# Kernel tuning notes

Measured on AMD Instinct MI355X. Metric: run time of the kernel, lower is better.

The kernel has to match this reference:

```python
import jax, jax.numpy as jnp
import numpy as np

B, N, IN_C, HID, K1, K2, OUT_C = 128, 512, 128, 32, 100, 10, 10
E_PER = 8192  # edges per graph (avg degree 16)
EPS = 1e-15


def _lin(key, fan_in, fan_out):
    return jax.random.normal(key, (fan_in, fan_out), jnp.float32) / np.sqrt(fan_in)


def setup_inputs() -> dict:
    key = jax.random.key(0)
    ks = jax.random.split(key, 20)
    total = B * N
    x = jax.random.normal(ks[0], (total, IN_C), jnp.float32)
    # per-graph random edges, offset into the global node index space
    src_l = jax.random.randint(ks[1], (B, E_PER), 0, N)
    dst_l = jax.random.randint(ks[2], (B, E_PER), 0, N)
    off = (jnp.arange(B, dtype=jnp.int32) * N)[:, None]
    edge_index = jnp.stack([(src_l + off).reshape(-1), (dst_l + off).reshape(-1)]).astype(jnp.int32)
    batch = (jnp.arange(total, dtype=jnp.int32) // N).astype(jnp.int32)
    return {
        "x": x,
        "edge_index": edge_index,
        "batch": batch,
        "conv1_W": _lin(ks[3], IN_C, HID), "conv1_b": jnp.zeros((HID,), jnp.float32),
        "pool1_W": _lin(ks[4], HID, K1), "pool1_b": jnp.zeros((K1,), jnp.float32),
        "conv2_rel_W": _lin(ks[5], HID, HID), "conv2_rel_b": jnp.zeros((HID,), jnp.float32),
        "conv2_root_W": _lin(ks[6], HID, HID),
        "pool2_W": _lin(ks[7], HID, K2), "pool2_b": jnp.zeros((K2,), jnp.float32),
        "conv3_rel_W": _lin(ks[8], HID, HID), "conv3_rel_b": jnp.zeros((HID,), jnp.float32),
        "conv3_root_W": _lin(ks[9], HID, HID),
        "lin1_W": _lin(ks[10], HID, HID), "lin1_b": jnp.zeros((HID,), jnp.float32),
        "lin2_W": _lin(ks[11], HID, OUT_C), "lin2_b": jnp.zeros((OUT_C,), jnp.float32),
    }


def gcn_conv(x, edge_index, W, b):
    # GCNConv with add_self_loops=True, symmetric normalization
    total = x.shape[0]
    loops = jnp.arange(total, dtype=edge_index.dtype)
    src = jnp.concatenate([edge_index[0], loops])
    dst = jnp.concatenate([edge_index[1], loops])
    w = jnp.ones(src.shape[0], x.dtype)
    deg = jax.ops.segment_sum(w, dst, num_segments=total)
    dis = jnp.where(deg > 0, jax.lax.rsqrt(deg), 0.0)
    norm = dis[src] * dis[dst]
    xw = x @ W
    out = jax.ops.segment_sum(norm[:, None] * xw[src], dst, num_segments=total)
    return out + b


def dense_mincut_pool(x, adj, s, mask=None):
    # x:[b,n,f] adj:[b,n,n] s:[b,n,k]
    s = jax.nn.softmax(s, axis=-1)
    if mask is not None:
        m = mask[..., None].astype(x.dtype)
        x = x * m
        s = s * m
    out = jnp.einsum('bnk,bnf->bkf', s, x)
    out_adj = jnp.einsum('bnk,bnm,bml->bkl', s, adj, s)
    mincut_num = jnp.trace(out_adj, axis1=-2, axis2=-1)
    d_flat = adj.sum(-1)  # [b,n]
    mincut_den = jnp.einsum('bnk,bn,bnk->b', s, d_flat, s)  # trace(s^T D s)
    mincut_loss = jnp.mean(-(mincut_num / mincut_den))
    k = s.shape[-1]
    ss = jnp.einsum('bnk,bnl->bkl', s, s)
    ss_norm = jnp.linalg.norm(ss, axis=(-1, -2), keepdims=True)
    i_s = jnp.eye(k, dtype=x.dtype) / jnp.sqrt(jnp.asarray(k, x.dtype))  # I_k / ||I_k||_F
    ortho_loss = jnp.mean(jnp.linalg.norm(ss / ss_norm - i_s, axis=(-1, -2)))
    # zero diagonal then symmetric degree-normalize
    out_adj = out_adj * (1.0 - jnp.eye(k, dtype=x.dtype))
    d = jnp.sqrt(out_adj.sum(-1))[..., None] + EPS
    out_adj = out_adj / d / jnp.swapaxes(d, -1, -2)
    return out, out_adj, mincut_loss, ortho_loss


def dense_graph_conv(x, adj, rel_W, rel_b, root_W):
    # DenseGraphConv(aggr='add'): lin_rel(adj @ x) + lin_root(x)
    return (adj @ x) @ rel_W + rel_b + x @ root_W


def reference(x, edge_index, batch, conv1_W, conv1_b, pool1_W, pool1_b,
              conv2_rel_W, conv2_rel_b, conv2_root_W, pool2_W, pool2_b,
              conv3_rel_W, conv3_rel_b, conv3_root_W, lin1_W, lin1_b, lin2_W, lin2_b):
    h = jax.nn.relu(gcn_conv(x, edge_index, conv1_W, conv1_b))
    # to_dense_batch: sorted batch with N nodes per graph -> reshape; mask all-true
    xd = h.reshape(B, N, HID)
    mask = jnp.ones((B, N), bool)
    # to_dense_adj
    b_idx = edge_index[0] // N
    s_l = edge_index[0] % N
    d_l = edge_index[1] % N
    adj = jnp.zeros((B, N, N), x.dtype).at[b_idx, s_l, d_l].add(1.0)
    s = xd @ pool1_W + pool1_b
    xd, adj, mc1, o1 = dense_mincut_pool(xd, adj, s, mask)
    xd = jax.nn.relu(dense_graph_conv(xd, adj, conv2_rel_W, conv2_rel_b, conv2_root_W))
    s = xd @ pool2_W + pool2_b
    xd, adj, mc2, o2 = dense_mincut_pool(xd, adj, s)
    xd = dense_graph_conv(xd, adj, conv3_rel_W, conv3_rel_b, conv3_root_W)
    g = xd.mean(axis=1)  # [B, HID]
    g = jax.nn.relu(g @ lin1_W + lin1_b)
    g = g @ lin2_W + lin2_b
    return jax.nn.log_softmax(g, axis=-1), mc1 + mc2 + o1 + o2
```

## Files before the change

kernel.cpp:

```cpp
#include <hip/hip_runtime.h>
#include <hip/hip_bf16.h>

#define TB   128
#define NN   512
#define INC  128
#define HH   32
#define KP1  100
#define KP2  10
#define OC   10
#define EPER 8192
#define NT   (TB*NN)
#define ET   (TB*EPER)
#define ZTR  264
#define ZTS  40
#define XTS  136

typedef unsigned int  u32;
typedef unsigned short u16;
typedef __attribute__((ext_vector_type(8))) short bf16x8;
typedef __attribute__((ext_vector_type(16))) float f32x16;

__device__ __forceinline__ u32 bfr(float f) {
    u32 b = __float_as_uint(f);
    return (b + 0x7fffu + ((b >> 16) & 1u)) >> 16;
}
__device__ __forceinline__ u32 pk2(float a, float b) { return bfr(a) | (bfr(b) << 16); }
__device__ __forceinline__ float blo(u32 u) { return __uint_as_float(u << 16); }
__device__ __forceinline__ float bhi(u32 u) { return __uint_as_float(u & 0xffff0000u); }

__global__ __launch_bounds__(1024) void k_pre(const int* __restrict__ ei,
                                              int* __restrict__ cnt_src, int* __restrict__ cnt_dst,
                                              int* __restrict__ off_src, int* __restrict__ off_dst,
                                              u16* __restrict__ srt_dst, u16* __restrict__ srt_src,
                                              float* __restrict__ dis, float* __restrict__ aux,
                                              const float* __restrict__ x, const float* __restrict__ W,
                                              u16* __restrict__ xwb, float* __restrict__ out) {
    __shared__ __align__(16) u16 sX[512 * XTS];
    __shared__ __align__(16) u16 sW[32 * XTS];
    int tid = threadIdx.x, b = blockIdx.x;
    if (b < TB) {
        int* hs = (int*)sX;
        int* hd = hs + NN;
        int* ps = hd + NN;
        int* pd = ps + NN;
        u16* sdl = (u16*)(pd + NN);
        u16* ssl = sdl + EPER;
        int g = b, goff = g * NN;
        if (tid == 0) aux[g] = 0.f;
        if (g == 0 && tid == 0) out[1280] = 0.f;
        if (tid < NN) { hs[tid] = 0; hd[tid] = 0; }
        __syncthreads();
        const int* es = ei + (size_t)g * EPER;
        const int* ed = ei + ET + (size_t)g * EPER;
        for (int e = tid; e < EPER; e += 1024) {
            atomicAdd(&hs[es[e] - goff], 1);
            atomicAdd(&hd[ed[e] - goff], 1);
        }
        __syncthreads();
        int vs = 0, vd = 0;
        if (tid < NN) { vs = hs[tid]; vd = hd[tid]; ps[tid] = vs; pd[tid] = vd; }
        __syncthreads();
        for (int off = 1; off < NN; off <<= 1) {
            int xa = 0, xb = 0;
            if (tid < NN) {
                xa = ps[tid]; xb = pd[tid];
                if (tid >= off) { xa += ps[tid - off]; xb += pd[tid - off]; }
            }
            __syncthreads();
            if (tid < NN) { ps[tid] = xa; pd[tid] = xb; }
            __syncthreads();
        }
        int eso = 0, edo = 0;
        if (tid < NN) {
            eso = ps[tid] - vs; edo = pd[tid] - vd;
            cnt_src[goff + tid] = vs;  cnt_dst[goff + tid] = vd;
            off_src[goff + tid] = g * EPER + eso;
            off_dst[goff + tid] = g * EPER + edo;
            dis[goff + tid] = rsqrtf(1.0f + (float)vd);
        }
        __syncthreads();
        if (tid < NN) { ps[tid] = eso; pd[tid] = edo; }
        __syncthreads();
        for (int e = tid; e < EPER; e += 1024) {
            int s = es[e] - goff, d = ed[e] - goff;
            int p = atomicAdd(&ps[s], 1); sdl[p] = (u16)d;
            int q = atomicAdd(&pd[d], 1); ssl[q] = (u16)s;
        }
        __syncthreads();
        u32* wd = (u32*)(srt_dst + (size_t)g * EPER);
        u32* ws = (u32*)(srt_src + (size_t)g * EPER);
        const u32* rd = (const u32*)sdl;
        const u32* rs = (const u32*)ssl;
        for (int i = tid; i < EPER / 2; i += 1024) { wd[i] = rd[i]; ws[i] = rs[i]; }
        return;
    }
    int nbase = (b - TB) * 512;
    for (int i = tid; i < INC * HH; i += 1024) {
        int k = i >> 5, n = i & 31;
        sW[n * XTS + k] = (u16)bfr(W[i]);
    }
    for (int i = tid; i < 512 * 32; i += 1024) {
        int r = i >> 5, q = i & 31;
        float4 v = ((const float4*)(x + (size_t)(nbase + r) * INC))[q];
        u32* dst = (u32*)&sX[r * XTS + q * 4];
        dst[0] = pk2(v.x, v.y);
        dst[1] = pk2(v.z, v.w);
    }
    __syncthreads();
    int wave = tid >> 6, lane = tid & 63;
    int lc = lane & 31, half = lane >> 5;
    f32x16 acc;
#pragma unroll
    for (int r = 0; r < 16; r++) acc[r] = 0.f;
#pragma unroll
    for (int kc = 0; kc < 8; kc++) {
        bf16x8 af  = *(const bf16x8*)&sX[(wave * 32 + lc) * XTS + kc * 16 + half * 8];
        bf16x8 bfv = *(const bf16x8*)&sW[lc * XTS + kc * 16 + half * 8];
        acc = __builtin_amdgcn_mfma_f32_32x32x16_bf16(af, bfv, acc, 0, 0, 0);
    }
#pragma unroll
    for (int r = 0; r < 16; r++) {
        int m = (r & 3) + 8 * (r >> 2) + 4 * half;
        int rowg = nbase + wave * 32 + m;
        xwb[(size_t)rowg * HH + lc] = (u16)bfr(acc[r]);
    }
}

__global__ __launch_bounds__(256) void k_gcng(const u16* __restrict__ ssrc, const int* __restrict__ od,
                                              const int* __restrict__ cd, const u32* __restrict__ xwb32,
                                              const float* __restrict__ dis, const float* __restrict__ bias,
                                              u32* __restrict__ hb32) {
    int tid = threadIdx.x;
    int b = blockIdx.x;
    int r8 = b & 7, j = b >> 3;
    int g = r8 + 8 * (j & 15);
    int chunk = j >> 4;
    int n = g * NN + chunk * 16 + (tid >> 4), cp = tid & 15;
    int goff = g * NN;
    int base = od[n], cnt = cd[n];
    float dn = dis[n];
    u32 us = xwb32[(size_t)n * 16 + cp];
    float a0 = dn * blo(us), a1 = dn * bhi(us);
    int i = 0;
    for (; i + 4 <= cnt; i += 4) {
        int s0 = goff + ssrc[base + i],     s1v = goff + ssrc[base + i + 1];
        int s2 = goff + ssrc[base + i + 2], s3  = goff + ssrc[base + i + 3];
        float d0 = dis[s0], d1 = dis[s1v], d2 = dis[s2], d3 = dis[s3];
        u32 u0 = xwb32[(size_t)s0 * 16 + cp];
        u32 u1 = xwb32[(size_t)s1v * 16 + cp];
        u32 u2 = xwb32[(size_t)s2 * 16 + cp];
        u32 u3 = xwb32[(size_t)s3 * 16 + cp];
        a0 += d0 * blo(u0) + d1 * blo(u1) + d2 * blo(u2) + d3 * blo(u3);
        a1 += d0 * bhi(u0) + d1 * bhi(u1) + d2 * bhi(u2) + d3 * bhi(u3);
    }
    for (; i < cnt; i++) {
        int s0 = goff + ssrc[base + i]; float d0 = dis[s0];
        u32 u0 = xwb32[(size_t)s0 * 16 + cp];
        a0 += d0 * blo(u0); a1 += d0 * bhi(u0);
    }
    float v0 = fmaxf(dn * a0 + bias[2 * cp], 0.f);
    float v1 = fmaxf(dn * a1 + bias[2 * cp + 1], 0.f);
    hb32[(size_t)n * 16 + cp] = pk2(v0, v1);
}

__global__ __launch_bounds__(256) void k_s1m(const u32* __restrict__ hb32, const float* __restrict__ W,
                                             const float* __restrict__ bias, const int* __restrict__ csrc,
                                             u16* __restrict__ s1b, float* __restrict__ den1) {
    __shared__ u16 sH[128 * ZTS];
    __shared__ u16 sW[128 * ZTS];
    int tid = threadIdx.x;
    int nbase = blockIdx.x * 128;
    for (int i = tid; i < HH * KP1; i += 256) {
        int k = i / KP1, n = i - k * KP1;
        sW[n * ZTS + k] = (u16)bfr(W[i]);
    }
    for (int i = tid; i < 28 * 16; i += 256) {
        int n = 100 + (i >> 4), q = i & 15;
        ((u32*)sW)[n * (ZTS / 2) + q] = 0;
    }
    for (int i = tid; i < 128 * 16; i += 256) {
        int r = i >> 4, q = i & 15;
        ((u32*)sH)[r * (ZTS / 2) + q] = hb32[(size_t)(nbase + r) * 16 + q];
    }
    __syncthreads();
    int wave = tid >> 6, lane = tid & 63;
    int lc = lane & 31, half = lane >> 5;
    f32x16 acc[4];
#pragma unroll
    for (int t = 0; t < 4; t++)
#pragma unroll
        for (int r = 0; r < 16; r++) acc[t][r] = 0.f;
#pragma unroll
    for (int kc = 0; kc < 2; kc++) {
        bf16x8 af = *(const bf16x8*)&sH[(wave * 32 + lc) * ZTS + kc * 16 + half * 8];
#pragma unroll
        for (int t = 0; t < 4; t++) {
            bf16x8 bfv = *(const bf16x8*)&sW[(t * 32 + lc) * ZTS + kc * 16 + half * 8];
            acc[t] = __builtin_amdgcn_mfma_f32_32x32x16_bf16(af, bfv, acc[t], 0, 0, 0);
        }
    }
    float s[16], q[16];
#pragma unroll
    for (int r = 0; r < 16; r++) { s[r] = 0.f; q[r] = 0.f; }
#pragma unroll
    for (int t = 0; t < 4; t++) {
        int ch = t * 32 + lc;
        bool valid = ch < KP1;
        float bv = valid ? bias[ch] : 0.f;
#pragma unroll
        for (int r = 0; r < 16; r++) {
            float ev = valid ? __expf(acc[t][r] + bv) : 0.f;
            acc[t][r] = ev; s[r] += ev; q[r] = fmaf(ev, ev, q[r]);
        }
    }
#pragma unroll
    for (int off = 16; off >= 1; off >>= 1) {
#pragma unroll
        for (int r = 0; r < 16; r++) { s[r] += __shfl_xor(s[r], off); q[r] += __shfl_xor(q[r], off); }
    }
    float inv[16];
#pragma unroll
    for (int r = 0; r < 16; r++) inv[r] = 1.f / s[r];
#pragma unroll
    for (int t = 0; t < 4; t++) {
        int ch = t * 32 + lc;
        if (ch < KP1) {
#pragma unroll
            for (int r = 0; r < 16; r++) {
                int lr = (r & 3) + 8 * (r >> 2) + 4 * half;
                int rowg = nbase + wave * 32 + lr;
                s1b[(size_t)rowg * KP1 + ch] = (u16)bfr(acc[t][r] * inv[r]);
            }
        }
    }
    float contrib = 0.f;
    if (lc == 0) {
#pragma unroll
        for (int r = 0; r < 16; r++) {
            int lr = (r & 3) + 8 * (r >> 2) + 4 * half;
            int rowg = nbase + wave * 32 + lr;
            contrib += (float)csrc[rowg] * q[r] * inv[r] * inv[r];
        }
    }
    contrib += __shfl_xor(contrib, 32);
    if (lane == 0) atomicAdd(&den1[nbase >> 9], contrib);
}

__global__ __launch_bounds__(256) void k_t1g(const u16* __restrict__ sdst, const int* __restrict__ osr,
                                             const int* __restrict__ csr, const u32* __restrict__ s1b32,
                                             u32* __restrict__ t1b32) {
    int tid = threadIdx.x;
    int b = blockIdx.x;
    int r8 = b & 7, j = b >> 3;
    int g = r8 + 8 * (j & 15);
    int chunk = j >> 4;
    int n = g * NN + chunk * 4 + (tid >> 6), lane = tid & 63;
    if (lane >= 50) return;
    int goff = g * NN;
    int base = osr[n], cnt = csr[n];
    float a0 = 0.f, a1 = 0.f;
    int i = 0;
    for (; i + 4 <= cnt; i += 4) {
        int d0 = goff + sdst[base + i],     d1 = goff + sdst[base + i + 1];
        int d2 = goff + sdst[base + i + 2], d3 = goff + sdst[base + i + 3];
        u32 u0 = s1b32[(size_t)d0 * 50 + lane];
        u32 u1 = s1b32[(size_t)d1 * 50 + lane];
        u32 u2 = s1b32[(size_t)d2 * 50 + lane];
        u32 u3 = s1b32[(size_t)d3 * 50 + lane];
        a0 += (blo(u0) + blo(u1)) + (blo(u2) + blo(u3));
        a1 += (bhi(u0) + bhi(u1)) + (bhi(u2) + bhi(u3));
    }
    for (; i < cnt; i++) {
        int d0 = goff + sdst[base + i];
        u32 u0 = s1b32[(size_t)d0 * 50 + lane];
        a0 += blo(u0); a1 += bhi(u0);
    }
    t1b32[(size_t)n * 50 + lane] = pk2(a0, a1);
}

__device__ __forceinline__ void ld_cp(const u32* __restrict__ sp, int rstr,
                                      u32& w0, u32& w1, u32& w2, u32& w3) {
    w0 = sp[0]; w1 = sp[rstr]; w2 = sp[2 * rstr]; w3 = sp[3 * rstr];
}
__device__ __forceinline__ void st_cp(u16* __restrict__ zb, int doff,
                                      u32 w0, u32 w1, u32 w2, u32 w3) {
    u32 lo01 = (w0 & 0xffffu) | (w1 << 16);
    u32 lo23 = (w2 & 0xffffu) | (w3 << 16);
    u32 hi01 = (w0 >> 16) | (w1 & 0xffff0000u);
    u32 hi23 = (w2 >> 16) | (w3 & 0xffff0000u);
    *(uint2*)&zb[doff]       = make_uint2(lo01, lo23);
    *(uint2*)&zb[doff + ZTS] = make_uint2(hi01, hi23);
}

#define GRAM_MFMA(zb)                                                                               \
    {                                                                                               \
        bf16x8 af0 = *(const bf16x8*)&(zb)[(132 + (2*mtb    )*32 + lc)*ZTS + mfh*16 + half*8];      \
        bf16x8 af1 = *(const bf16x8*)&(zb)[(132 + (2*mtb + 1)*32 + lc)*ZTS + mfh*16 + half*8];      \
        bf16x8 bv0 = *(const bf16x8*)&(zb)[((2*ctb    )*32 + lc)*ZTS + mfh*16 + half*8];            \
        bf16x8 bv1 = *(const bf16x8*)&(zb)[((2*ctb + 1)*32 + lc)*ZTS + mfh*16 + half*8];            \
        acc00 = __builtin_amdgcn_mfma_f32_32x32x16_bf16(af0, bv0, acc00, 0, 0, 0);                  \
        acc01 = __builtin_amdgcn_mfma_f32_32x32x16_bf16(af0, bv1, acc01, 0, 0, 0);                  \
        acc10 = __builtin_amdgcn_mfma_f32_32x32x16_bf16(af1, bv0, acc10, 0, 0, 0);                  \
        acc11 = __builtin_amdgcn_mfma_f32_32x32x16_bf16(af1, bv1, acc11, 0, 0, 0);                  \
    }

#define DUMP_TILE(AV, MT, CT, ADD)                                                                  \
    {                                                                                               \
        int l = (CT) * 32 + lc;                                                                     \
        if (l < 232) {                                                                              \
            _Pragma("unroll")                                                                       \
            for (int r = 0; r < 16; r++) {                                                          \
                int k = (MT) * 32 + (r & 3) + 8 * (r >> 2) + 4 * half;                              \
                if (k < KP1) {                                                                      \
                    if (ADD) sC[k * 232 + l] += AV[r];                                              \
                    else     sC[k * 232 + l] = AV[r];                                               \
                }                                                                                   \
            }                                                                                       \
        }                                                                                           \
    }

__global__ __launch_bounds__(1024, 1) void k_gram2(const u32* __restrict__ s1b32, const u32* __restrict__ t1b32,
                                                   const u32* __restrict__ hb32, const float* __restrict__ aux,
                                                   const float* __restrict__ relW, const float* __restrict__ relB,
                                                   const float* __restrict__ rootW,
                                                   const float* __restrict__ p2W, const float* __restrict__ p2B,
                                                   const float* __restrict__ relW3, const float* __restrict__ relb3,
                                                   const float* __restrict__ rootW3,
                                                   const float* __restrict__ l1W, const float* __restrict__ l1b,
                                                   const float* __restrict__ l2W, const float* __restrict__ l2b,
                                                   float* __restrict__ out) {
    __shared__ __align__(16) u16 sZ[2][ZTR * ZTS];
    __shared__ float sC[KP1 * 232];
    __shared__ float sRow[KP1], sd[KP1];
    __shared__ float sScal[3];
    __shared__ float sL1;
    int g = blockIdx.x;
    int nbase = g * NN;
    int tid = threadIdx.x;
    int wave = tid >> 6, lane = tid & 63;
    int mfh = wave & 1;
    int mtb = (wave >> 1) & 1;
    int ctb = wave >> 2;
    int lc = lane & 31, half = lane >> 5;

    float* ov  = (float*)sZ;
    float* sXo = ov;
    float* sYo = ov + 3200;
    float* sS2 = ov + 6400;
    float* sT2 = ov + 7400;
    float* sA2 = ov + 8400;
    float* sB2 = ov + 8500;
    float* red = ov + 8600;
    float* sP2 = ov + 8700;
    float* sY3 = ov + 9020;
    float* sAn = ov + 9340;
    float* sG  = ov + 9440;
    float* sG1 = ov + 9472;
    float* sL  = ov + 9504;
    float* sdd = ov + 9514;
    float* sLse = ov + 9524;

    f32x16 acc00, acc01, acc10, acc11;
#pragma unroll
    for (int r = 0; r < 16; r++) { acc00[r] = 0.f; acc01[r] = 0.f; acc10[r] = 0.f; acc11[r] = 0.f; }

    int cp = (tid & 7) + ((tid >> 6) << 3);
    int rq = (tid >> 3) & 7;
    bool act = cp < 116;
    const u32* sp;
    int rstr;
    if (cp < 50)      { sp = t1b32 + cp;        rstr = 50; }
    else if (cp < 66) { sp = hb32 + (cp - 50);  rstr = 16; }
    else              { sp = s1b32 + (cp - 66); rstr = 50; }
    sp += (size_t)(nbase + rq * 4) * rstr;
    int step = rstr * 32;
    int doff = (2 * cp) * ZTS + rq * 4;

    if (tid < KP1) sRow[tid] = 0.f;
    if (tid < 3) sScal[tid] = 0.f;
    for (int i = tid; i < 32 * ZTS; i += 1024) {
        int r = 232 + i / ZTS, c = i % ZTS;
        sZ[0][r * ZTS + c] = 0; sZ[1][r * ZTS + c] = 0;
    }
    u32 a0, a1, a2, a3, b0 = 0, b1 = 0, b2 = 0, b3 = 0;
    if (act) {
        ld_cp(sp, rstr, a0, a1, a2, a3);
        st_cp(sZ[0], doff, a0, a1, a2, a3);
        sp += step;
        ld_cp(sp, rstr, b0, b1, b2, b3);
        sp += step;
    }
    __syncthreads();

    for (int nt = 0; nt < 16; nt += 2) {
        GRAM_MFMA(sZ[0]);
        if (act) {
            st_cp(sZ[1], doff, b0, b1, b2, b3);
            if (nt + 2 < 16) { ld_cp(sp, rstr, a0, a1, a2, a3); sp += step; }
        }
        __syncthreads();
        GRAM_MFMA(sZ[1]);
        if (act && nt + 2 < 16) {
            st_cp(sZ[0], doff, a0, a1, a2, a3);
            if (nt + 3 < 16) { ld_cp(sp, rstr, b0, b1, b2, b3); sp += step; }
        }
        __syncthreads();
    }
    if (mfh == 0) {
        DUMP_TILE(acc00, 2 * mtb,     2 * ctb,     0)
        DUMP_TILE(acc01, 2 * mtb,     2 * ctb + 1, 0)
        DUMP_TILE(acc10, 2 * mtb + 1, 2 * ctb,     0)
        DUMP_TILE(acc11, 2 * mtb + 1, 2 * ctb + 1, 0)
    }
    __syncthreads();
    if (mfh == 1) {
        DUMP_TILE(acc00, 2 * mtb,     2 * ctb,     1)
        DUMP_TILE(acc01, 2 * mtb,     2 * ctb + 1, 1)
        DUMP_TILE(acc10, 2 * mtb + 1, 2 * ctb,     1)
        DUMP_TILE(acc11, 2 * mtb + 1, 2 * ctb + 1, 1)
    }
    __syncthreads();
    {
        float ssq = 0.f, trss = 0.f, troa = 0.f;
        for (int idx = tid; idx < KP1 * 58; idx += 1024) {
            int k = idx / 58, q = idx - k * 58;
            float4 s = *(const float4*)&sC[k * 232 + q * 4];
            int c = q * 4;
            if (c < 100) {
                float rs = (s.x + s.y) + (s.z + s.w);
                if (k >= c && k < c + 4) { float d = ((const float*)&s)[k - c]; troa += d; rs -= d; }
                atomicAdd(&sRow[k], rs);
            } else if (c >= 132) {
                ssq += s.x * s.x + s.y * s.y + s.z * s.z + s.w * s.w;
                int l0 = c - 132;
                if (k >= l0 && k < l0 + 4) trss += ((const float*)&s)[k - l0];
            }
        }
#pragma unroll
        for (int off = 32; off >= 1; off >>= 1) {
            ssq  += __shfl_xor(ssq, off);
            trss += __shfl_xor(trss, off);
            troa += __shfl_xor(troa, off);
        }
        if ((tid & 63) == 0) {
            atomicAdd(&sScal[0], troa);
            atomicAdd(&sScal[1], trss);
            atomicAdd(&sScal[2], ssq);
        }
    }
    __syncthreads();
    if (tid == 0) {
        float o1 = sqrtf(fmaxf(2.f - 2.f * sScal[1] / (sqrtf(sScal[2]) * 10.f), 0.f));
        sL1 = -(sScal[0] / aux[g]) + o1;
    }
    if (tid < KP1) sd[tid] = sqrtf(sRow[tid]) + 1e-15f;
    __syncthreads();
    for (int i = tid; i < KP1 * KP1; i += 1024) {
        int k = i / KP1, l = i - k * KP1;
        float v = sC[k * 232 + l];
        sC[k * 232 + l] = (k == l) ? 0.f : v / (sd[k] * sd[l]);
    }
    for (int i = tid; i < KP1 * HH; i += 1024) {
        int k = i >> 5, c = i & 31;
        sXo[i] = sC[k * 232 + 100 + c];
    }
    if (tid < 32) sG[tid] = 0.f;
    __syncthreads();

    int n = tid >> 2, cq = tid & 3;
    if (tid < 400) {
        float yv[8];
#pragma unroll
        for (int j = 0; j < 8; j++) yv[j] = 0.f;
        for (int mq = 0; mq < 25; mq++) {
            float4 a4 = *(const float4*)&sC[n * 232 + mq * 4];
            const float* xb = &sXo[(mq * 4) * HH + cq * 8];
            float aa[4] = {a4.x, a4.y, a4.z, a4.w};
#pragma unroll
            for (int mm = 0; mm < 4; mm++) {
                const float* xr = xb + mm * HH;
#pragma unroll
                for (int j = 0; j < 8; j++) yv[j] = fmaf(aa[mm], xr[j], yv[j]);
            }
        }
#pragma unroll
        for (int j = 0; j < 8; j++) sYo[n * HH + cq * 8 + j] = yv[j];
    }
    __syncthreads();
    float x2v[8];
    if (tid < 400) {
#pragma unroll
        for (int j = 0; j < 8; j++) x2v[j] = relB[cq * 8 + j];
        for (int j = 0; j < 32; j++) {
            float yj = sYo[n * HH + j];
            float xj = sXo[n * HH + j];
            float4 r0 = *(const float4*)&relW[j * 32 + cq * 8];
            float4 r1v = *(const float4*)&relW[j * 32 + cq * 8 + 4];
            float4 q0 = *(const float4*)&rootW[j * 32 + cq * 8];
            float4 q1 = *(const float4*)&rootW[j * 32 + cq * 8 + 4];
            x2v[0] += yj * r0.x + xj * q0.x;  x2v[1] += yj * r0.y + xj * q0.y;
            x2v[2] += yj * r0.z + xj * q0.z;  x2v[3] += yj * r0.w + xj * q0.w;
            x2v[4] += yj * r1v.x + xj * q1.x; x2v[5] += yj * r1v.y + xj * q1.y;
            x2v[6] += yj * r1v.z + xj * q1.z; x2v[7] += yj * r1v.w + xj * q1.w;
        }
    }
    __syncthreads();
    if (tid < 400) {
#pragma unroll
        for (int j = 0; j < 8; j++) sXo[n * HH + cq * 8 + j] = fmaxf(x2v[j], 0.f);
    }
    __syncthreads();
    if (tid < KP1) {
        float lg[10];
#pragma unroll
        for (int j = 0; j < 10; j++) lg[j] = p2B[j];
        for (int c = 0; c < 32; c++) {
            float xv = sXo[tid * HH + c];
#pragma unroll
            for (int j = 0; j < 10; j++) lg[j] = fmaf(xv, p2W[c * 10 + j], lg[j]);
        }
        float mx = lg[0];
#pragma unroll
        for (int j = 1; j < 10; j++) mx = fmaxf(mx, lg[j]);
        float se = 0.f;
#pragma unroll
        for (int j = 0; j < 10; j++) { lg[j] = __expf(lg[j] - mx); se += lg[j]; }
        float inv = 1.f / se, sq = 0.f;
#pragma unroll
        for (int j = 0; j < 10; j++) { float sv = lg[j] * inv; sS2[tid * 10 + j] = sv; sq += sv * sv; }
        float d2 = 0.f;
        for (int mq = 0; mq < 25; mq++) {
            float4 a4 = *(const float4*)&sC[tid * 232 + mq * 4];
            d2 += a4.x + a4.y + a4.z + a4.w;
        }
        red[tid] = d2 * sq;
    }
    __syncthreads();
    for (int p = tid; p < KP1 * KP2; p += 1024) {
        int n2 = p / 10, jj = p % 10;
        float a = 0.f;
        for (int m = 0; m < KP1; m++) a = fmaf(sC[n2 * 232 + m], sS2[m * 10 + jj], a);
        sT2[p] = a;
    }
    if (tid < KP2 * HH) {
        int k = tid >> 5, cc = tid & 31;
        float a = 0.f;
        for (int n2 = 0; n2 < KP1; n2++) a = fmaf(sS2[n2 * 10 + k], sXo[n2 * HH + cc], a);
        sP2[tid] = a;
    }
    __syncthreads();
    if (tid < 100) {
        int k = tid / 10, l = tid % 10;
        float oa = 0.f, ss = 0.f;
        for (int n2 = 0; n2 < KP1; n2++) {
            float sk = sS2[n2 * 10 + k];
            oa = fmaf(sk, sT2[n2 * 10 + l], oa);
            ss = fmaf(sk, sS2[n2 * 10 + l], ss);
        }
        sA2[tid] = oa; sB2[tid] = ss;
    }
    __syncthreads();
    if (tid == 0) {
        float den2 = 0.f;
        for (int i = 0; i < 100; i++) den2 += red[i];
        float troa = 0.f, trss = 0.f, ssq = 0.f;
        for (int k = 0; k < 10; k++) { troa += sA2[k * 10 + k]; trss += sB2[k * 10 + k]; }
        for (int i = 0; i < 100; i++) ssq += sB2[i] * sB2[i];
        float o2 = sqrtf(fmaxf(2.f - 2.f * trss / (sqrtf(ssq) * 3.16227766f), 0.f));
        float l2 = -(troa / den2) + o2;
        atomicAdd(&out[1280], (sL1 + l2) * (1.f / 128.f));
    }
    if (tid < 10) {
        float rs = 0.f;
        for (int l = 0; l < 10; l++) if (l != tid) rs += sA2[tid * 10 + l];
        sdd[tid] = sqrtf(rs) + 1e-15f;
    }
    __syncthreads();
    if (tid < 100) {
        int k = tid / 10, l = tid % 10;
        sAn[tid] = (k == l) ? 0.f : sA2[tid] / (sdd[k] * sdd[l]);
    }
    __syncthreads();
    if (tid < KP2 * HH) {
        int k = tid >> 5, cc = tid & 31;
        float a = 0.f;
#pragma unroll
        for (int m = 0; m < 10; m++) a = fmaf(sAn[k * 10 + m], sP2[m * HH + cc], a);
        sY3[tid] = a;
    }
    __syncthreads();
    if (tid < KP2 * HH) {
        int k = tid >> 5, cc = tid & 31;
        float v = relb3[cc];
        for (int j = 0; j < 32; j++)
            v += sY3[k * HH + j] * relW3[j * 32 + cc] + sP2[k * HH + j] * rootW3[j * 32 + cc];
        atomicAdd(&sG[cc], v * 0.1f);
    }
    __syncthreads();
    if (tid < 32) {
        float v = l1b[tid];
        for (int j = 0; j < 32; j++) v = fmaf(sG[j], l1W[j * 32 + tid], v);
        sG1[tid] = fmaxf(v, 0.f);
    }
    __syncthreads();
    if (tid < 10) {
        float v = l2b[tid];
        for (int j = 0; j < 32; j++) v = fmaf(sG1[j], l2W[j * 10 + tid], v);
        sL[tid] = v;
    }
    __syncthreads();
    if (tid == 0) {
        float mx = sL[0];
        for (int j = 1; j < 10; j++) mx = fmaxf(mx, sL[j]);
        float se = 0.f;
        for (int j = 0; j < 10; j++) se += expf(sL[j] - mx);
        *sLse = mx + logf(se);
    }
    __syncthreads();
    if (tid < 10) out[(size_t)g * 10 + tid] = sL[tid] - *sLse;
}

extern "C" void kernel_launch(void* const* d_in, const int* in_sizes, int n_in,
                              void* d_out, int out_size, void* d_ws, size_t ws_size,
                              hipStream_t stream) {
    const float* x    = (const float*)d_in[0];
    const int*   ei   = (const int*)d_in[1];
    const float* c1W  = (const float*)d_in[3];
    const float* c1b  = (const float*)d_in[4];
    const float* p1W  = (const float*)d_in[5];
    const float* p1b  = (const float*)d_in[6];
    const float* relW2  = (const float*)d_in[7];
    const float* relb2  = (const float*)d_in[8];
    const float* rootW2 = (const float*)d_in[9];
    const float* p2W  = (const float*)d_in[10];
    const float* p2b  = (const float*)d_in[11];
    const float* relW3  = (const float*)d_in[12];
    const float* relb3  = (const float*)d_in[13];
    const float* rootW3 = (const float*)d_in[14];
    const float* l1W  = (const float*)d_in[15];
    const float* l1b  = (const float*)d_in[16];
    const float* l2W  = (const float*)d_in[17];
    const float* l2b  = (const float*)d_in[18];
    float* out = (float*)d_out;

    int*  cnt_src = (int*)d_ws;
    int*  cnt_dst = cnt_src + NT;
    int*  off_src = cnt_dst + NT;
    int*  off_dst = off_src + NT;
    u16*  srt_dst = (u16*)(off_dst + NT);
    u16*  srt_src = srt_dst + ET;
    float* dis = (float*)(srt_src + ET);
    u32*  xwb  = (u32*)(dis + NT);
    u32*  hb   = xwb + (size_t)NT * 16;
    u32*  s1b  = hb + (size_t)NT * 16;
    u32*  t1b  = s1b + (size_t)NT * 50;
    float* aux  = (float*)(t1b + (size_t)NT * 50);

    k_pre<<<2 * TB, 1024, 0, stream>>>(ei, cnt_src, cnt_dst, off_src, off_dst,
                                       srt_dst, srt_src, dis, aux, x, c1W, (u16*)xwb, out);
    k_gcng<<<NT / 16, 256, 0, stream>>>(srt_src, off_dst, cnt_dst, xwb, dis, c1b, hb);
    k_s1m<<<NT / 128, 256, 0, stream>>>(hb, p1W, p1b, cnt_src, (u16*)s1b, aux );
    k_t1g<<<NT / 4, 256, 0, stream>>>(srt_dst, off_src, cnt_src, s1b, t1b);
    k_gram2<<<TB, 1024, 0, stream>>>(s1b, t1b, hb, aux, relW2, relb2, rootW2, p2W, p2b,
                                     relW3, relb3, rootW3, l1W, l1b, l2W, l2b, out);
}
```

Baseline: 248.4 us.

## Split gram kernel over node halves with global partial reduction

The per-graph gram MFMA kernel is split into two blocks per graph, each covering half of the 512 nodes. Each block writes a partial 100x232 fp32 tile to a global workspace, and a new finalize kernel sums the two partials and runs the rest of the pooling, convolution and MLP pipeline. This doubles the grid from 128 to 256 blocks so more of the device's compute units are busy during the gram phase. In exchange it adds an extra kernel launch and roughly 24 MB of global writes and reads for the partial tiles.

```diff
diff --git a/kernel.cpp b/kernel.cpp
--- a/kernel.cpp
+++ b/kernel.cpp
@@ -14,6 +14,7 @@
 #define ZTR  264
 #define ZTS  40
 #define XTS  136
+#define CSZ  (KP1*232)
 
 typedef unsigned int  u32;
 typedef unsigned short u16;
@@ -319,23 +320,13 @@
         }                                                                                           \
     }
 
-__global__ __launch_bounds__(1024, 1) void k_gram2(const u32* __restrict__ s1b32, const u32* __restrict__ t1b32,
-                                                   const u32* __restrict__ hb32, const float* __restrict__ aux,
-                                                   const float* __restrict__ relW, const float* __restrict__ relB,
-                                                   const float* __restrict__ rootW,
-                                                   const float* __restrict__ p2W, const float* __restrict__ p2B,
-                                                   const float* __restrict__ relW3, const float* __restrict__ relb3,
-                                                   const float* __restrict__ rootW3,
-                                                   const float* __restrict__ l1W, const float* __restrict__ l1b,
-                                                   const float* __restrict__ l2W, const float* __restrict__ l2b,
-                                                   float* __restrict__ out) {
+__global__ __launch_bounds__(1024, 1) void k_gramA(const u32* __restrict__ s1b32, const u32* __restrict__ t1b32,
+                                                   const u32* __restrict__ hb32, float* __restrict__ Cp) {
     __shared__ __align__(16) u16 sZ[2][ZTR * ZTS];
-    __shared__ float sC[KP1 * 232];
-    __shared__ float sRow[KP1], sd[KP1];
-    __shared__ float sScal[3];
-    __shared__ float sL1;
-    int g = blockIdx.x;
-    int nbase = g * NN;
+    __shared__ float sC[CSZ];
+    int b = blockIdx.x;
+    int g = b & (TB - 1), kh = b >> 7;
+    int nbase = g * NN + kh * 256;
     int tid = threadIdx.x;
     int wave = tid >> 6, lane = tid & 63;
     int mfh = wave & 1;
@@ -343,7 +334,86 @@
     int ctb = wave >> 2;
     int lc = lane & 31, half = lane >> 5;
 
-    float* ov  = (float*)sZ;
+    f32x16 acc00, acc01, acc10, acc11;
+#pragma unroll
+    for (int r = 0; r < 16; r++) { acc00[r] = 0.f; acc01[r] = 0.f; acc10[r] = 0.f; acc11[r] = 0.f; }
+
+    int cp = (tid & 7) + ((tid >> 6) << 3);
+    int rq = (tid >> 3) & 7;
+    bool act = cp < 116;
+    const u32* sp;
+    int rstr;
+    if (cp < 50)      { sp = t1b32 + cp;        rstr = 50; }
+    else if (cp < 66) { sp = hb32 + (cp - 50);  rstr = 16; }
+    else              { sp = s1b32 + (cp - 66); rstr = 50; }
+    sp += (size_t)(nbase + rq * 4) * rstr;
+    int step = rstr * 32;
+    int doff = (2 * cp) * ZTS + rq * 4;
+
+    for (int i = tid; i < 32 * ZTS; i += 1024) {
+        int r = 232 + i / ZTS, c = i % ZTS;
+        sZ[0][r * ZTS + c] = 0; sZ[1][r * ZTS + c] = 0;
+    }
+    u32 a0, a1, a2, a3, b0 = 0, b1 = 0, b2 = 0, b3 = 0;
+    if (act) {
+        ld_cp(sp, rstr, a0, a1, a2, a3);
+        st_cp(sZ[0], doff, a0, a1, a2, a3);
+        sp += step;
+        ld_cp(sp, rstr, b0, b1, b2, b3);
+        sp += step;
+    }
+    __syncthreads();
+
+    for (int nt = 0; nt < 8; nt += 2) {
+        GRAM_MFMA(sZ[0]);
+        if (act) {
+            st_cp(sZ[1], doff, b0, b1, b2, b3);
+            if (nt + 2 < 8) { ld_cp(sp, rstr, a0, a1, a2, a3); sp += step; }
+        }
+        __syncthreads();
+        GRAM_MFMA(sZ[1]);
+        if (act && nt + 2 < 8) {
+            st_cp(sZ[0], doff, a0, a1, a2, a3);
+            if (nt + 3 < 8) { ld_cp(sp, rstr, b0, b1, b2, b3); sp += step; }
+        }
+        __syncthreads();
+    }
+    if (mfh == 0) {
+        DUMP_TILE(acc00, 2 * mtb,     2 * ctb,     0)
+        DUMP_TILE(acc01, 2 * mtb,     2 * ctb + 1, 0)
+        DUMP_TILE(acc10, 2 * mtb + 1, 2 * ctb,     0)
+        DUMP_TILE(acc11, 2 * mtb + 1, 2 * ctb + 1, 0)
+    }
+    __syncthreads();
+    if (mfh == 1) {
+        DUMP_TILE(acc00, 2 * mtb,     2 * ctb,     1)
+        DUMP_TILE(acc01, 2 * mtb,     2 * ctb + 1, 1)
+        DUMP_TILE(acc10, 2 * mtb + 1, 2 * ctb,     1)
+        DUMP_TILE(acc11, 2 * mtb + 1, 2 * ctb + 1, 1)
+    }
+    __syncthreads();
+    float4* dst = (float4*)(Cp + (size_t)b * CSZ);
+    const float4* src = (const float4*)sC;
+    for (int i = tid; i < CSZ / 4; i += 1024) dst[i] = src[i];
+}
+
+__global__ __launch_bounds__(1024, 1) void k_fin2(const float* __restrict__ Cp, const float* __restrict__ aux,
+                                                  const float* __restrict__ relW, const float* __restrict__ relB,
+                                                  const float* __restrict__ rootW,
+                                                  const float* __restrict__ p2W, const float* __restrict__ p2B,
+                                                  const float* __restrict__ relW3, const float* __restrict__ relb3,
+                                                  const float* __restrict__ rootW3,
+                                                  const float* __restrict__ l1W, const float* __restrict__ l1b,
+                                                  const float* __restrict__ l2W, const float* __restrict__ l2b,
+                                                  float* __restrict__ out) {
+    __shared__ float sC[CSZ];
+    __shared__ float ov[10560];
+    __shared__ float sRow[KP1], sd[KP1];
+    __shared__ float sScal[3];
+    __shared__ float sL1;
+    int g = blockIdx.x;
+    int tid = threadIdx.x;
+
     float* sXo = ov;
     float* sYo = ov + 3200;
     float* sS2 = ov + 6400;
@@ -360,64 +430,18 @@
     float* sdd = ov + 9514;
     float* sLse = ov + 9524;
 
-    f32x16 acc00, acc01, acc10, acc11;
-#pragma unroll
-    for (int r = 0; r < 16; r++) { acc00[r] = 0.f; acc01[r] = 0.f; acc10[r] = 0.f; acc11[r] = 0.f; }
-
-    int cp = (tid & 7) + ((tid >> 6) << 3);
-    int rq = (tid >> 3) & 7;
-    bool act = cp < 116;
-    const u32* sp;
-    int rstr;
-    if (cp < 50)      { sp = t1b32 + cp;        rstr = 50; }
-    else if (cp < 66) { sp = hb32 + (cp - 50);  rstr = 16; }
-    else              { sp = s1b32 + (cp - 66); rstr = 50; }
-    sp += (size_t)(nbase + rq * 4) * rstr;
-    int step = rstr * 32;
-    int doff = (2 * cp) * ZTS + rq * 4;
-
     if (tid < KP1) sRow[tid] = 0.f;
     if (tid < 3) sScal[tid] = 0.f;
-    for (int i = tid; i < 32 * ZTS; i += 1024) {
-        int r = 232 + i / ZTS, c = i % ZTS;
-        sZ[0][r * ZTS + c] = 0; sZ[1][r * ZTS + c] = 0;
-    }
-    u32 a0, a1, a2, a3, b0 = 0, b1 = 0, b2 = 0, b3 = 0;
-    if (act) {
-        ld_cp(sp, rstr, a0, a1, a2, a3);
-        st_cp(sZ[0], doff, a0, a1, a2, a3);
-        sp += step;
-        ld_cp(sp, rstr, b0, b1, b2, b3);
-        sp += step;
-    }
-    __syncthreads();
-
-    for (int nt = 0; nt < 16; nt += 2) {
-        GRAM_MFMA(sZ[0]);
-        if (act) {
-            st_cp(sZ[1], doff, b0, b1, b2, b3);
-            if (nt + 2 < 16) { ld_cp(sp, rstr, a0, a1, a2, a3); sp += step; }
-        }
-        __syncthreads();
-        GRAM_MFMA(sZ[1]);
-        if (act && nt + 2 < 16) {
-            st_cp(sZ[0], doff, a0, a1, a2, a3);
-            if (nt + 3 < 16) { ld_cp(sp, rstr, b0, b1, b2, b3); sp += step; }
-        }
-        __syncthreads();
-    }
-    if (mfh == 0) {
-        DUMP_TILE(acc00, 2 * mtb,     2 * ctb,     0)
-        DUMP_TILE(acc01, 2 * mtb,     2 * ctb + 1, 0)
-        DUMP_TILE(acc10, 2 * mtb + 1, 2 * ctb,     0)
-        DUMP_TILE(acc11, 2 * mtb + 1, 2 * ctb + 1, 0)
-    }
-    __syncthreads();
-    if (mfh == 1) {
-        DUMP_TILE(acc00, 2 * mtb,     2 * ctb,     1)
-        DUMP_TILE(acc01, 2 * mtb,     2 * ctb + 1, 1)
-        DUMP_TILE(acc10, 2 * mtb + 1, 2 * ctb,     1)
-        DUMP_TILE(acc11, 2 * mtb + 1, 2 * ctb + 1, 1)
+    if (tid < 32) sG[tid] = 0.f;
+    {
+        const float4* pa = (const float4*)(Cp + (size_t)g * CSZ);
+        const float4* pb = (const float4*)(Cp + (size_t)(g + TB) * CSZ);
+        float4* dst = (float4*)sC;
+        for (int i = tid; i < CSZ / 4; i += 1024) {
+            float4 a = pa[i], b = pb[i];
+            a.x += b.x; a.y += b.y; a.z += b.z; a.w += b.w;
+            dst[i] = a;
+        }
     }
     __syncthreads();
     {
@@ -464,7 +488,6 @@
         int k = i >> 5, c = i & 31;
         sXo[i] = sC[k * 232 + 100 + c];
     }
-    if (tid < 32) sG[tid] = 0.f;
     __syncthreads();
 
     int n = tid >> 2, cq = tid & 3;
@@ -654,13 +677,15 @@
     u32*  hb   = xwb + (size_t)NT * 16;
     u32*  s1b  = hb + (size_t)NT * 16;
     u32*  t1b  = s1b + (size_t)NT * 50;
-    float* aux  = (float*)(t1b + (size_t)NT * 50);
+    float* Cp   = (float*)(t1b + (size_t)NT * 50);
+    float* aux  = Cp + (size_t)2 * TB * CSZ;
 
     k_pre<<<2 * TB, 1024, 0, stream>>>(ei, cnt_src, cnt_dst, off_src, off_dst,
                                        srt_dst, srt_src, dis, aux, x, c1W, (u16*)xwb, out);
     k_gcng<<<NT / 16, 256, 0, stream>>>(srt_src, off_dst, cnt_dst, xwb, dis, c1b, hb);
     k_s1m<<<NT / 128, 256, 0, stream>>>(hb, p1W, p1b, cnt_src, (u16*)s1b, aux );
     k_t1g<<<NT / 4, 256, 0, stream>>>(srt_dst, off_src, cnt_src, s1b, t1b);
-    k_gram2<<<TB, 1024, 0, stream>>>(s1b, t1b, hb, aux, relW2, relb2, rootW2, p2W, p2b,
-                                     relW3, relb3, rootW3, l1W, l1b, l2W, l2b, out);
-}
+    k_gramA<<<2 * TB, 1024, 0, stream>>>(s1b, t1b, hb, Cp);
+    k_fin2<<<TB, 1024, 0, stream>>>(Cp, aux, relW2, relb2, rootW2, p2W, p2b,
+                                    relW3, relb3, rootW3, l1W, l1b, l2W, l2b, out);
+}
```

After: 253.7 us. 2.1% more time.
